# Optimization experiments

Hardware: AMD Instinct MI355X
Metric: run time of the kernel (lower is better)

Reference implementation:

```python
import jax, jax.numpy as jnp
import numpy as np


def setup_inputs() -> dict:
    key = jax.random.key(0)
    k1, k2 = jax.random.split(key)
    B, N = 2048, 2048
    y_prime = jax.random.normal(k1, (B, N, 3), dtype=jnp.float32)
    y = jax.random.normal(k2, (B, N, 3), dtype=jnp.float32)
    return {"y_prime": y_prime, "y": y}


def reference(y_prime, y):
    """Batched SVD-superimposer (Kabsch) RMSD, averaged over the batch.

    Faithful to Biopython's SVDSuperimposer as used by RMSDLoss:
      set(reference=y, coords=y_prime); run(); get_rms().
    """
    n_atoms = y.shape[1]
    # Center both point clouds (av1/av2 in SVDSuperimposer)
    c = y_prime - jnp.mean(y_prime, axis=1, keepdims=True)  # coords, [B,N,3]
    r = y - jnp.mean(y, axis=1, keepdims=True)              # reference, [B,N,3]
    # a = coords^T @ reference  -> [B,3,3]
    a = jnp.einsum('bni,bnj->bij', c, r)
    u, s, vt = jnp.linalg.svd(a, full_matrices=False)
    # rot = (vt^T u^T)^T = u @ vt; fix improper rotation (reflection) via det sign
    det = jnp.linalg.det(jnp.einsum('bik,bkj->bij', u, vt))  # [B]
    sign = jnp.sign(det)
    ones = jnp.ones_like(sign)
    flip = jnp.stack([ones, ones, sign], axis=-1)            # [B,3]
    rot = jnp.einsum('bik,bk,bkj->bij', u, flip, vt)         # [B,3,3]
    # transformed = centered_coords @ rot; compare to centered reference
    diff = jnp.einsum('bni,bij->bnj', c, rot) - r
    rms = jnp.sqrt(jnp.sum(diff * diff, axis=(1, 2)) / n_atoms)  # [B]
    return jnp.mean(rms)
```

## Files before the change

### kernel.cpp

```cpp
#include <hip/hip_runtime.h>
#include <cmath>


constexpr int BLOCK = 256;
constexpr int NWAVE = BLOCK / 64;

__global__ __launch_bounds__(BLOCK) void rmsd_per_batch(
    const float* __restrict__ yp,
    const float* __restrict__ yr,
    float* __restrict__ rms_out,
    int n)
{
    const int b   = blockIdx.x;
    const int tid = threadIdx.x;
    const size_t row = (size_t)b * (size_t)n * 3u;
    const float4* p4 = (const float4*)(yp + row);
    const float4* r4 = (const float4*)(yr + row);

    float s1x=0.f,s1y=0.f,s1z=0.f, s2x=0.f,s2y=0.f,s2z=0.f, sq1=0.f,sq2=0.f;
    float c00=0.f,c01=0.f,c02=0.f,c10=0.f,c11=0.f,c12=0.f,c20=0.f,c21=0.f,c22=0.f;

    const int ngroups = n >> 2;
    for (int g = tid; g < ngroups; g += BLOCK) {
        float4 a0 = p4[g*3+0], a1 = p4[g*3+1], a2 = p4[g*3+2];
        float4 b0 = r4[g*3+0], b1 = r4[g*3+1], b2 = r4[g*3+2];
        float px[4]={a0.x,a0.w,a1.z,a2.y};
        float py[4]={a0.y,a1.x,a1.w,a2.z};
        float pz[4]={a0.z,a1.y,a2.x,a2.w};
        float qx[4]={b0.x,b0.w,b1.z,b2.y};
        float qy[4]={b0.y,b1.x,b1.w,b2.z};
        float qz[4]={b0.z,b1.y,b2.x,b2.w};
        #pragma unroll
        for (int k=0;k<4;k++){
            s1x+=px[k]; s1y+=py[k]; s1z+=pz[k];
            s2x+=qx[k]; s2y+=qy[k]; s2z+=qz[k];
            sq1 = fmaf(px[k],px[k], fmaf(py[k],py[k], fmaf(pz[k],pz[k], sq1)));
            sq2 = fmaf(qx[k],qx[k], fmaf(qy[k],qy[k], fmaf(qz[k],qz[k], sq2)));
            c00=fmaf(px[k],qx[k],c00); c01=fmaf(px[k],qy[k],c01); c02=fmaf(px[k],qz[k],c02);
            c10=fmaf(py[k],qx[k],c10); c11=fmaf(py[k],qy[k],c11); c12=fmaf(py[k],qz[k],c12);
            c20=fmaf(pz[k],qx[k],c20); c21=fmaf(pz[k],qy[k],c21); c22=fmaf(pz[k],qz[k],c22);
        }
    }

    float vals[17] = {s1x,s1y,s1z,s2x,s2y,s2z,sq1,sq2,
                      c00,c01,c02,c10,c11,c12,c20,c21,c22};
    __shared__ float sred[NWAVE][17];
    const int wave = tid >> 6, lane = tid & 63;
    #pragma unroll
    for (int i=0;i<17;i++){
        float v = vals[i];
        #pragma unroll
        for (int off=32; off>0; off>>=1) v += __shfl_down(v, off, 64);
        if (lane==0) sred[wave][i] = v;
    }
    __syncthreads();

    if (tid == 0) {
        double t[17];
        #pragma unroll
        for (int i=0;i<17;i++){
            double s = 0.0;
            #pragma unroll
            for (int w=0;w<NWAVE;w++) s += (double)sred[w][i];
            t[i] = s;
        }
        const double dn = (double)n;
        const double m1[3] = {t[0]/dn, t[1]/dn, t[2]/dn};
        const double m2[3] = {t[3]/dn, t[4]/dn, t[5]/dn};
        const double E0 =
            (t[6] - dn*(m1[0]*m1[0]+m1[1]*m1[1]+m1[2]*m1[2])) +
            (t[7] - dn*(m2[0]*m2[0]+m2[1]*m2[1]+m2[2]*m2[2]));
        double A[3][3];
        A[0][0]=t[8] -dn*m1[0]*m2[0]; A[0][1]=t[9] -dn*m1[0]*m2[1]; A[0][2]=t[10]-dn*m1[0]*m2[2];
        A[1][0]=t[11]-dn*m1[1]*m2[0]; A[1][1]=t[12]-dn*m1[1]*m2[1]; A[1][2]=t[13]-dn*m1[1]*m2[2];
        A[2][0]=t[14]-dn*m1[2]*m2[0]; A[2][1]=t[15]-dn*m1[2]*m2[1]; A[2][2]=t[16]-dn*m1[2]*m2[2];

        const double det =
              A[0][0]*(A[1][1]*A[2][2]-A[1][2]*A[2][1])
            - A[0][1]*(A[1][0]*A[2][2]-A[1][2]*A[2][0])
            + A[0][2]*(A[1][0]*A[2][1]-A[1][1]*A[2][0]);

        double B00=0,B01=0,B02=0,B11=0,B12=0,B22=0;
        #pragma unroll
        for (int k=0;k<3;k++){
            B00 += A[k][0]*A[k][0]; B01 += A[k][0]*A[k][1]; B02 += A[k][0]*A[k][2];
            B11 += A[k][1]*A[k][1]; B12 += A[k][1]*A[k][2]; B22 += A[k][2]*A[k][2];
        }
        const double q  = (B00+B11+B22)/3.0;
        const double p1 = B01*B01 + B02*B02 + B12*B12;
        const double p2 = (B00-q)*(B00-q)+(B11-q)*(B11-q)+(B22-q)*(B22-q) + 2.0*p1;
        const double p  = sqrt(p2/6.0);
        double e1, e2, e3;
        if (p < 1e-300) {
            e1 = e2 = e3 = q;
        } else {
            const double C00=(B00-q)/p, C01=B01/p, C02=B02/p;
            const double C11=(B11-q)/p, C12=B12/p, C22=(B22-q)/p;
            double detC = C00*(C11*C22-C12*C12)
                        - C01*(C01*C22-C12*C02)
                        + C02*(C01*C12-C11*C02);
            double rr = detC * 0.5;
            rr = fmin(1.0, fmax(-1.0, rr));
            const double phi = acos(rr)/3.0;
            e1 = q + 2.0*p*cos(phi);
            e3 = q + 2.0*p*cos(phi + 2.0943951023931953);
            e2 = 3.0*q - e1 - e3;
        }
        const double s0 = sqrt(fmax(e1,0.0));
        const double s1 = sqrt(fmax(e2,0.0));
        const double s2 = sqrt(fmax(e3,0.0));
        const double dsign = (det >= 0.0) ? 1.0 : -1.0;
        const double trs = s0 + s1 + dsign*s2;
        const double msd = fmax(0.0, (E0 - 2.0*trs)/dn);
        rms_out[b] = (float)sqrt(msd);
    }
}

__global__ __launch_bounds__(BLOCK) void mean_kernel(
    const float* __restrict__ rms, float* __restrict__ out, int B)
{
    const int tid = threadIdx.x;
    float s = 0.f;
    for (int i = tid; i < B; i += BLOCK) s += rms[i];
    #pragma unroll
    for (int off=32; off>0; off>>=1) s += __shfl_down(s, off, 64);
    __shared__ float sred[NWAVE];
    const int wave = tid >> 6, lane = tid & 63;
    if (lane==0) sred[wave] = s;
    __syncthreads();
    if (tid == 0) {
        float tot = 0.f;
        #pragma unroll
        for (int w=0; w<NWAVE; w++) tot += sred[w];
        out[0] = tot / (float)B;
    }
}

extern "C" void kernel_launch(void* const* d_in, const int* in_sizes, int n_in,
                              void* d_out, int out_size, void* d_ws, size_t ws_size,
                              hipStream_t stream) {
    const float* yp = (const float*)d_in[0];
    const float* yr = (const float*)d_in[1];
    const int N = 2048;
    const int B = in_sizes[0] / (N * 3);
    float* rms_ws = (float*)d_ws;

    rmsd_per_batch<<<B, BLOCK, 0, stream>>>(yp, yr, rms_ws, N);
    mean_kernel<<<1, BLOCK, 0, stream>>>(rms_ws, (float*)d_out, B);
}
```

Measured before the change: 30.56 us.

## Split per-batch stats from the eigen solve and do the solve in fp32

The per-batch kernel now only reduces the 17 sufficient statistics and writes them in a struct-of-arrays layout. A single-block second kernel then runs the 3x3 Kabsch/eigenvalue solve for all batches in float and averages the RMS values. This removes the serial fp64 tail (acos, cos, sqrt on one thread) from each of the 2048 streaming blocks. The cost is that the single-block solve serializes 2048 solves across 256 threads. Using fp32 throughout also risks precision loss, since E0 and the cross terms are formed by cancellation.

```diff
diff --git a/kernel.cpp b/kernel.cpp
--- a/kernel.cpp
+++ b/kernel.cpp
@@ -4,12 +4,13 @@
 
 constexpr int BLOCK = 256;
 constexpr int NWAVE = BLOCK / 64;
+constexpr int NS = 17;
 
-__global__ __launch_bounds__(BLOCK) void rmsd_per_batch(
+__global__ __launch_bounds__(BLOCK) void stats_kernel(
     const float* __restrict__ yp,
     const float* __restrict__ yr,
-    float* __restrict__ rms_out,
-    int n)
+    float* __restrict__ stats,
+    int n, int B)
 {
     const int b   = blockIdx.x;
     const int tid = threadIdx.x;
@@ -42,12 +43,12 @@
         }
     }
 
-    float vals[17] = {s1x,s1y,s1z,s2x,s2y,s2z,sq1,sq2,
+    float vals[NS] = {s1x,s1y,s1z,s2x,s2y,s2z,sq1,sq2,
                       c00,c01,c02,c10,c11,c12,c20,c21,c22};
-    __shared__ float sred[NWAVE][17];
+    __shared__ float sred[NWAVE][NS];
     const int wave = tid >> 6, lane = tid & 63;
     #pragma unroll
-    for (int i=0;i<17;i++){
+    for (int i=0;i<NS;i++){
         float v = vals[i];
         #pragma unroll
         for (int off=32; off>0; off>>=1) v += __shfl_down(v, off, 64);
@@ -55,78 +56,79 @@
     }
     __syncthreads();
 
-    if (tid == 0) {
-        double t[17];
+    if (tid < NS) {
+        float s = 0.f;
         #pragma unroll
-        for (int i=0;i<17;i++){
-            double s = 0.0;
-            #pragma unroll
-            for (int w=0;w<NWAVE;w++) s += (double)sred[w][i];
-            t[i] = s;
-        }
-        const double dn = (double)n;
-        const double m1[3] = {t[0]/dn, t[1]/dn, t[2]/dn};
-        const double m2[3] = {t[3]/dn, t[4]/dn, t[5]/dn};
-        const double E0 =
-            (t[6] - dn*(m1[0]*m1[0]+m1[1]*m1[1]+m1[2]*m1[2])) +
-            (t[7] - dn*(m2[0]*m2[0]+m2[1]*m2[1]+m2[2]*m2[2]));
-        double A[3][3];
-        A[0][0]=t[8] -dn*m1[0]*m2[0]; A[0][1]=t[9] -dn*m1[0]*m2[1]; A[0][2]=t[10]-dn*m1[0]*m2[2];
-        A[1][0]=t[11]-dn*m1[1]*m2[0]; A[1][1]=t[12]-dn*m1[1]*m2[1]; A[1][2]=t[13]-dn*m1[1]*m2[2];
-        A[2][0]=t[14]-dn*m1[2]*m2[0]; A[2][1]=t[15]-dn*m1[2]*m2[1]; A[2][2]=t[16]-dn*m1[2]*m2[2];
-
-        const double det =
-              A[0][0]*(A[1][1]*A[2][2]-A[1][2]*A[2][1])
-            - A[0][1]*(A[1][0]*A[2][2]-A[1][2]*A[2][0])
-            + A[0][2]*(A[1][0]*A[2][1]-A[1][1]*A[2][0]);
-
-        double B00=0,B01=0,B02=0,B11=0,B12=0,B22=0;
-        #pragma unroll
-        for (int k=0;k<3;k++){
-            B00 += A[k][0]*A[k][0]; B01 += A[k][0]*A[k][1]; B02 += A[k][0]*A[k][2];
-            B11 += A[k][1]*A[k][1]; B12 += A[k][1]*A[k][2]; B22 += A[k][2]*A[k][2];
-        }
-        const double q  = (B00+B11+B22)/3.0;
-        const double p1 = B01*B01 + B02*B02 + B12*B12;
-        const double p2 = (B00-q)*(B00-q)+(B11-q)*(B11-q)+(B22-q)*(B22-q) + 2.0*p1;
-        const double p  = sqrt(p2/6.0);
-        double e1, e2, e3;
-        if (p < 1e-300) {
-            e1 = e2 = e3 = q;
-        } else {
-            const double C00=(B00-q)/p, C01=B01/p, C02=B02/p;
-            const double C11=(B11-q)/p, C12=B12/p, C22=(B22-q)/p;
-            double detC = C00*(C11*C22-C12*C12)
-                        - C01*(C01*C22-C12*C02)
-                        + C02*(C01*C12-C11*C02);
-            double rr = detC * 0.5;
-            rr = fmin(1.0, fmax(-1.0, rr));
-            const double phi = acos(rr)/3.0;
-            e1 = q + 2.0*p*cos(phi);
-            e3 = q + 2.0*p*cos(phi + 2.0943951023931953);
-            e2 = 3.0*q - e1 - e3;
-        }
-        const double s0 = sqrt(fmax(e1,0.0));
-        const double s1 = sqrt(fmax(e2,0.0));
-        const double s2 = sqrt(fmax(e3,0.0));
-        const double dsign = (det >= 0.0) ? 1.0 : -1.0;
-        const double trs = s0 + s1 + dsign*s2;
-        const double msd = fmax(0.0, (E0 - 2.0*trs)/dn);
-        rms_out[b] = (float)sqrt(msd);
+        for (int w=0;w<NWAVE;w++) s += sred[w][tid];
+        stats[tid * B + b] = s;
     }
 }
 
-__global__ __launch_bounds__(BLOCK) void mean_kernel(
-    const float* __restrict__ rms, float* __restrict__ out, int B)
+__global__ __launch_bounds__(BLOCK) void solve_kernel(
+    const float* __restrict__ stats,
+    float* __restrict__ out, int n, int B)
 {
     const int tid = threadIdx.x;
-    float s = 0.f;
-    for (int i = tid; i < B; i += BLOCK) s += rms[i];
+    const float fn = (float)n;
+    float acc = 0.f;
+
+    for (int b = tid; b < B; b += BLOCK) {
+        float t[NS];
+        #pragma unroll
+        for (int i=0;i<NS;i++) t[i] = stats[i*B + b];
+
+        const float m1x=t[0]/fn, m1y=t[1]/fn, m1z=t[2]/fn;
+        const float m2x=t[3]/fn, m2y=t[4]/fn, m2z=t[5]/fn;
+        const float E0 = (t[6] - fn*(m1x*m1x+m1y*m1y+m1z*m1z))
+                       + (t[7] - fn*(m2x*m2x+m2y*m2y+m2z*m2z));
+        const float A00=t[8] -fn*m1x*m2x, A01=t[9] -fn*m1x*m2y, A02=t[10]-fn*m1x*m2z;
+        const float A10=t[11]-fn*m1y*m2x, A11=t[12]-fn*m1y*m2y, A12=t[13]-fn*m1y*m2z;
+        const float A20=t[14]-fn*m1z*m2x, A21=t[15]-fn*m1z*m2y, A22=t[16]-fn*m1z*m2z;
+
+        const float det = A00*(A11*A22-A12*A21)
+                        - A01*(A10*A22-A12*A20)
+                        + A02*(A10*A21-A11*A20);
+
+        const float G00 = A00*A00+A10*A10+A20*A20;
+        const float G01 = A00*A01+A10*A11+A20*A21;
+        const float G02 = A00*A02+A10*A12+A20*A22;
+        const float G11 = A01*A01+A11*A11+A21*A21;
+        const float G12 = A01*A02+A11*A12+A21*A22;
+        const float G22 = A02*A02+A12*A12+A22*A22;
+
+        const float q  = (G00+G11+G22)*(1.f/3.f);
+        const float p1 = G01*G01 + G02*G02 + G12*G12;
+        const float p2 = (G00-q)*(G00-q)+(G11-q)*(G11-q)+(G22-q)*(G22-q) + 2.f*p1;
+        const float p  = sqrtf(p2*(1.f/6.f));
+        float e1, e2, e3;
+        if (p < 1e-20f) {
+            e1 = e2 = e3 = q;
+        } else {
+            const float ip = 1.f/p;
+            const float C00=(G00-q)*ip, C01=G01*ip, C02=G02*ip;
+            const float C11=(G11-q)*ip, C12=G12*ip, C22=(G22-q)*ip;
+            float detC = C00*(C11*C22-C12*C12)
+                       - C01*(C01*C22-C12*C02)
+                       + C02*(C01*C12-C11*C02);
+            float rr = fminf(1.f, fmaxf(-1.f, 0.5f*detC));
+            const float phi = acosf(rr)*(1.f/3.f);
+            e1 = q + 2.f*p*cosf(phi);
+            e3 = q + 2.f*p*cosf(phi + 2.0943951023931953f);
+            e2 = 3.f*q - e1 - e3;
+        }
+        const float s0 = sqrtf(fmaxf(e1,0.f));
+        const float s1 = sqrtf(fmaxf(e2,0.f));
+        const float s2 = sqrtf(fmaxf(e3,0.f));
+        const float trs = s0 + s1 + ((det >= 0.f) ? s2 : -s2);
+        const float msd = fmaxf(0.f, (E0 - 2.f*trs)/fn);
+        acc += sqrtf(msd);
+    }
+
     #pragma unroll
-    for (int off=32; off>0; off>>=1) s += __shfl_down(s, off, 64);
+    for (int off=32; off>0; off>>=1) acc += __shfl_down(acc, off, 64);
     __shared__ float sred[NWAVE];
     const int wave = tid >> 6, lane = tid & 63;
-    if (lane==0) sred[wave] = s;
+    if (lane==0) sred[wave] = acc;
     __syncthreads();
     if (tid == 0) {
         float tot = 0.f;
@@ -143,8 +145,8 @@
     const float* yr = (const float*)d_in[1];
     const int N = 2048;
     const int B = in_sizes[0] / (N * 3);
-    float* rms_ws = (float*)d_ws;
+    float* stats_ws = (float*)d_ws;
 
-    rmsd_per_batch<<<B, BLOCK, 0, stream>>>(yp, yr, rms_ws, N);
-    mean_kernel<<<1, BLOCK, 0, stream>>>(rms_ws, (float*)d_out, B);
+    stats_kernel<<<B, BLOCK, 0, stream>>>(yp, yr, stats_ws, N, B);
+    solve_kernel<<<1, BLOCK, 0, stream>>>(stats_ws, (float*)d_out, N, B);
 }
```

Result: slower. 34.48 us (+12.8%).
